# Kernel optimization log

Measured on AMD Instinct MI355X. Metric: run time of the kernel, lower is better.

The kernel has to match this reference:

```python
import jax, jax.numpy as jnp
import numpy as np

N = 32768      # total nodes = 256 graphs x 128 nodes
G = 256        # graphs in batch
NPG = 128      # nodes per graph
DEG = 8        # incoming edges per node
E = N * DEG    # 262144 edges
F_IN = 64      # node feature size
F_E = 16       # edge feature size
EMB = 64       # out_channels per head == embedding_size
H = 4          # attention heads
HC = H * EMB   # 256
DENSE = 256
K = 64         # ceil(0.5 * NPG)
EPS = 1e-5


def setup_inputs() -> dict:
    key = jax.random.key(0)
    ks = list(jax.random.split(key, 32))
    it = iter(ks)
    s = 0.05

    def rn(shape):
        return jax.random.normal(next(it), shape, jnp.float32) * s

    x = jax.random.normal(next(it), (N, F_IN), jnp.float32)
    dst = jnp.repeat(jnp.arange(N, dtype=jnp.int32), DEG)
    src = (dst // NPG) * NPG + jax.random.randint(next(it), (E,), 0, NPG, dtype=jnp.int32)
    edge_index = jnp.stack([src, dst])                      # [2, E], edges stay within graph
    edge_attr = jax.random.normal(next(it), (E, F_E), jnp.float32)
    batch_index = jnp.arange(N, dtype=jnp.int32) // NPG

    inp = dict(
        x=x, edge_index=edge_index, edge_attr=edge_attr, batch_index=batch_index,
        # TransformerConv 1 (in=F_IN)
        Wq1=rn((F_IN, HC)), bq1=jnp.zeros((HC,), jnp.float32),
        Wk1=rn((F_IN, HC)), bk1=jnp.zeros((HC,), jnp.float32),
        Wv1=rn((F_IN, HC)), bv1=jnp.zeros((HC,), jnp.float32),
        We1=rn((F_E, HC)),
        Ws1=rn((F_IN, HC)), bs1=jnp.zeros((HC,), jnp.float32),
        Wb1=rn((3 * HC, 1)),
        t1_W=rn((HC, EMB)), t1_b=jnp.zeros((EMB,), jnp.float32),
        bn1_g=jnp.ones((EMB,), jnp.float32), bn1_b=jnp.zeros((EMB,), jnp.float32),
        # TransformerConv 2 (in=EMB)
        Wq2=rn((EMB, HC)), bq2=jnp.zeros((HC,), jnp.float32),
        Wk2=rn((EMB, HC)), bk2=jnp.zeros((HC,), jnp.float32),
        Wv2=rn((EMB, HC)), bv2=jnp.zeros((HC,), jnp.float32),
        We2=rn((F_E, HC)),
        Ws2=rn((EMB, HC)), bs2=jnp.zeros((HC,), jnp.float32),
        Wb2=rn((3 * HC, 1)),
        t2_W=rn((HC, EMB)), t2_b=jnp.zeros((EMB,), jnp.float32),
        bn2_g=jnp.ones((EMB,), jnp.float32), bn2_b=jnp.zeros((EMB,), jnp.float32),
        # TopKPooling + MLP head
        pool_w=rn((EMB,)),
        l1_W=rn((2 * EMB, DENSE)), l1_b=jnp.zeros((DENSE,), jnp.float32),
        l2_W=rn((DENSE, DENSE // 2)), l2_b=jnp.zeros((DENSE // 2,), jnp.float32),
        l3_W=rn((DENSE // 2, 1)), l3_b=jnp.zeros((1,), jnp.float32),
    )
    return inp


def _tconv(x, src, dst, ea, Wq, bq, Wk, bk, Wv, bv, We, Ws, bs, Wb):
    """PyG TransformerConv with edge_dim, beta=True, concat=True."""
    n = x.shape[0]
    q = (x @ Wq + bq).reshape(n, H, EMB)                    # [N,H,C]
    eemb = (ea @ We).reshape(-1, H, EMB)                    # [E,H,C]
    k = (x @ Wk + bk)[src].reshape(-1, H, EMB) + eemb       # edge features added to key
    v = (x @ Wv + bv)[src].reshape(-1, H, EMB) + eemb       # and to value
    alpha = jnp.einsum('ehc,ehc->eh', q[dst], k) / jnp.sqrt(jnp.float32(EMB))  # [E,H]
    # stable segment softmax over incoming edges of each dst node
    amax = jax.ops.segment_max(alpha, dst, num_segments=n)
    pexp = jnp.exp(alpha - amax[dst])
    denom = jax.ops.segment_sum(pexp, dst, num_segments=n)
    attn = pexp / denom[dst]                                # [E,H]
    out = jax.ops.segment_sum(v * attn[..., None], dst, num_segments=n).reshape(n, HC)
    # beta gated skip: lin_skip(x) and lin_beta([out, xr, out-xr])
    xr = x @ Ws + bs
    beta = jax.nn.sigmoid(jnp.concatenate([out, xr, out - xr], axis=-1) @ Wb)  # [N,1]
    return beta * xr + (1.0 - beta) * out


def _bn(x, g, b):
    m = x.mean(0)
    v = x.var(0)
    return g * (x - m) * jax.lax.rsqrt(v + EPS) + b


def _forward(x, edge_attr,
             Wq1, bq1, Wk1, bk1, Wv1, bv1, We1, Ws1, bs1, Wb1, t1_W, t1_b, bn1_g, bn1_b,
             Wq2, bq2, Wk2, bk2, Wv2, bv2, We2, Ws2, bs2, Wb2, t2_W, t2_b, bn2_g, bn2_b,
             pool_w, l1_W, l1_b, l2_W, l2_b, l3_W, l3_b,
             edge_index, batch_index):
    src, dst = edge_index[0], edge_index[1]
    h = _tconv(x, src, dst, edge_attr, Wq1, bq1, Wk1, bk1, Wv1, bv1, We1, Ws1, bs1, Wb1)
    h = _bn(jax.nn.relu(h @ t1_W + t1_b), bn1_g, bn1_b)
    h = _tconv(h, src, dst, edge_attr, Wq2, bq2, Wk2, bk2, Wv2, bv2, We2, Ws2, bs2, Wb2)
    h = _bn(jax.nn.relu(h @ t2_W + t2_b), bn2_g, bn2_b)
    # TopKPooling: score = (x.w)/||w||, keep top K per graph, scale by tanh(score)
    score = (h @ pool_w) / jnp.linalg.norm(pool_w)          # [N]
    sv, si = jax.lax.top_k(score.reshape(G, NPG), K)        # [G,K]
    xs = jnp.take_along_axis(h.reshape(G, NPG, EMB), si[..., None], axis=1)  # [G,K,EMB]
    xs = xs * jnp.tanh(sv)[..., None]
    # readout: global max pool || global mean pool
    rep = jnp.concatenate([xs.max(axis=1), xs.mean(axis=1)], axis=-1)  # [G, 2*EMB]
    hd = jax.nn.relu(rep @ l1_W + l1_b)
    hd = jax.nn.relu(hd @ l2_W + l2_b)
    return hd @ l3_W + l3_b                                  # [G,1]


def reference(x, edge_index, edge_attr, batch_index,
              Wq1, bq1, Wk1, bk1, Wv1, bv1, We1, Ws1, bs1, Wb1, t1_W, t1_b, bn1_g, bn1_b,
              Wq2, bq2, Wk2, bk2, Wv2, bv2, We2, Ws2, bs2, Wb2, t2_W, t2_b, bn2_g, bn2_b,
              pool_w, l1_W, l1_b, l2_W, l2_b, l3_W, l3_b):
    return _forward(x, edge_attr,
                    Wq1, bq1, Wk1, bk1, Wv1, bv1, We1, Ws1, bs1, Wb1, t1_W, t1_b, bn1_g, bn1_b,
                    Wq2, bq2, Wk2, bk2, Wv2, bv2, We2, Ws2, bs2, Wb2, t2_W, t2_b, bn2_g, bn2_b,
                    pool_w, l1_W, l1_b, l2_W, l2_b, l3_W, l3_b,
                    edge_index, batch_index)
```

## Files before the change

### kernel.cpp

```cpp
#include <hip/hip_runtime.h>
#include <math.h>

#define NN 32768
#define NG 256
#define DEG 8
#define HC 256
#define NCAT 1088
#define HCP 320
#define KTOP 64
#define EPSBN 1e-5f

typedef __attribute__((ext_vector_type(8))) short short8v;
typedef __attribute__((ext_vector_type(4))) float f32x4;

__device__ inline float bf2f(unsigned short u) {
    union { unsigned int i; float f; } c; c.i = ((unsigned int)u) << 16; return c.f;
}
__device__ inline unsigned short f2bf(float f) {
    union { float f; unsigned int i; } c; c.f = f;
    unsigned int r = c.i + 0x7FFFu + ((c.i >> 16) & 1u);
    return (unsigned short)(r >> 16);
}
__device__ inline void split2(float v, unsigned short& hi, unsigned short& lo) {
    hi = f2bf(v);
    union { float f; unsigned int i; } c; c.f = v - bf2f(hi);
    lo = (unsigned short)(c.i >> 16);
}
__device__ inline int permcol(int n) {
    if (n < 256 || n >= 768) return n;
    if (n < 512) { int l = n - 256; return 256 + ((l >> 2) << 3) + (l & 3); }
    int l = n - 512; return 256 + ((l >> 2) << 3) + 4 + (l & 3);
}

__device__ void prep_dev(int b, int t,
    const float* __restrict__ Wq, const float* __restrict__ bq,
    const float* __restrict__ Wk, const float* __restrict__ bk,
    const float* __restrict__ Wv, const float* __restrict__ bv,
    const float* __restrict__ Ws, const float* __restrict__ bs,
    const float* __restrict__ We, const float* __restrict__ tW,
    const float* __restrict__ Wb,
    unsigned short* __restrict__ WThi, unsigned short* __restrict__ WTlo,
    float* __restrict__ bcat,
    unsigned short* __restrict__ tWThi, unsigned short* __restrict__ tWTlo,
    float* __restrict__ Wbf, float* __restrict__ stats)
{
    if (b < 16) {
        int n = b * 64 + (t >> 2);
        int cc = n & 255;
        const float* src = (n < 256) ? Wq : (n < 512) ? Wk : (n < 768) ? Wv : Ws;
        int p = permcol(n);
        int k0 = (t & 3) * 16;
        #pragma unroll
        for (int k = k0; k < k0 + 16; k++) {
            unsigned short h, l;
            split2(src[k * 256 + cc], h, l);
            WThi[p * 64 + k] = h; WTlo[p * 64 + k] = l;
        }
    } else if (b < 32) {
        int idx = (b - 16) * 256 + t;
        int k = idx >> 6, o = idx & 63;
        int h = o >> 4, f = o & 15;
        const float* wq = Wq + k * 256 + h * 64;
        const float* we = We + f * 256 + h * 64;
        float s = 0.f;
        #pragma unroll
        for (int d = 0; d < 64; d++) s += wq[d] * we[d];
        unsigned short hh, ll;
        split2(s, hh, ll);
        WThi[(1024 + o) * 64 + k] = hh; WTlo[(1024 + o) * 64 + k] = ll;
    } else if (b < 48) {
        int idx = (b - 32) * 256 + t;
        int kp = idx >> 6, n = idx & 63;
        int h = kp >> 4, f = kp & 15;
        const float* we = We + f * 256 + h * 64;
        const float* tw = tW + (h * 64) * 64 + n;
        float s = 0.f;
        #pragma unroll
        for (int d = 0; d < 64; d++) s += we[d] * tw[d * 64];
        unsigned short hh, ll;
        split2(s, hh, ll);
        tWThi[n * HCP + 256 + kp] = hh; tWTlo[n * HCP + 256 + kp] = ll;
    } else if (b < 64) {
        int base = (b - 48) * 1024 + t * 4;
        #pragma unroll
        for (int i = 0; i < 4; i++) {
            int idx = base + i;
            int n = idx >> 8, k = idx & 255;
            unsigned short h, l;
            split2(tW[k * 64 + n], h, l);
            tWThi[n * HCP + k] = h; tWTlo[n * HCP + k] = l;
        }
    } else {
        if (t < 128) stats[t] = 0.f;
        Wbf[t]       = Wb[t]       + Wb[512 + t];
        Wbf[256 + t] = Wb[256 + t] - Wb[512 + t];
        for (int c = t; c < 1024; c += 256) {
            int cc = c & 255;
            float v = (c < 256) ? bq[cc] : (c < 512) ? bk[cc] : (c < 768) ? bv[cc] : bs[cc];
            bcat[permcol(c)] = v;
        }
        if (t < 64) {
            int h = t >> 4, f = t & 15;
            const float* we = We + f * 256 + h * 64;
            float s = 0.f, sb = 0.f;
            #pragma unroll
            for (int d = 0; d < 64; d++) {
                s  += we[d] * (Wb[h * 64 + d] + Wb[512 + h * 64 + d]);
                sb += we[d] * bq[h * 64 + d];
            }
            Wbf[512 + t] = s;
            bcat[1024 + t] = sb;
        }
    }
}

__global__ __launch_bounds__(256) void prep_all(
    const float* Wq1, const float* bq1, const float* Wk1, const float* bk1,
    const float* Wv1, const float* bv1, const float* Ws1, const float* bs1,
    const float* We1, const float* t1W, const float* Wb1,
    unsigned short* WThi1, unsigned short* WTlo1, float* bcat1,
    unsigned short* tWThi1, unsigned short* tWTlo1, float* Wbf1, float* stats1,
    const float* Wq2, const float* bq2, const float* Wk2, const float* bk2,
    const float* Wv2, const float* bv2, const float* Ws2, const float* bs2,
    const float* We2, const float* t2W, const float* Wb2,
    unsigned short* WThi2, unsigned short* WTlo2, float* bcat2,
    unsigned short* tWThi2, unsigned short* tWTlo2, float* Wbf2, float* stats2)
{
    const int b = blockIdx.x, t = threadIdx.x;
    if (b < 65)
        prep_dev(b, t, Wq1, bq1, Wk1, bk1, Wv1, bv1, Ws1, bs1, We1, t1W, Wb1,
                 WThi1, WTlo1, bcat1, tWThi1, tWTlo1, Wbf1, stats1);
    else
        prep_dev(b - 65, t, Wq2, bq2, Wk2, bk2, Wv2, bv2, Ws2, bs2, We2, t2W, Wb2,
                 WThi2, WTlo2, bcat2, tWThi2, tWTlo2, Wbf2, stats2);
}

__global__ __launch_bounds__(256) void proj_mfma(
    const float* __restrict__ A, const float* __restrict__ stats,
    const float* __restrict__ gbn, const float* __restrict__ bbn,
    const unsigned short* __restrict__ WThi, const unsigned short* __restrict__ WTlo,
    const float* __restrict__ bcat, unsigned short* __restrict__ C)
{
    __shared__ unsigned short AhiL[4096], AloL[4096];
    __shared__ unsigned short WhiL[4096], WloL[4096];
    __shared__ float CL[64 * 68];
    __shared__ float scl[64], sft[64];
    const int t = threadIdx.x;
    const int row0 = blockIdx.x * 64;
    const int w = t >> 6, l = t & 63;
    const int lr = l & 15, lg = l >> 4, ls = l & 7;

    if (t < 64) {
        if (stats) {
            float mean = stats[t] * (1.f / NN);
            float var  = stats[64 + t] * (1.f / NN) - mean * mean;
            float s = gbn[t] * rsqrtf(var + EPSBN);
            scl[t] = s; sft[t] = bbn[t] - mean * s;
        } else { scl[t] = 1.f; sft[t] = 0.f; }
    }
    __syncthreads();

    #pragma unroll
    for (int g = 0; g < 2; g++) {
        int idx = t * 8 + g * 2048;
        int r = idx >> 6, c = idx & 63;
        int ch = (c >> 3) ^ (r & 7);
        float4 a0 = *(const float4*)(A + (size_t)(row0 + r) * 64 + c);
        float4 a1 = *(const float4*)(A + (size_t)(row0 + r) * 64 + c + 4);
        float av[8] = {a0.x, a0.y, a0.z, a0.w, a1.x, a1.y, a1.z, a1.w};
        short8v vh, vl;
        #pragma unroll
        for (int j = 0; j < 8; j++) {
            float v = av[j] * scl[c + j] + sft[c + j];
            unsigned short h2, l2;
            split2(v, h2, l2);
            vh[j] = (short)h2; vl[j] = (short)l2;
        }
        *(short8v*)(AhiL + r * 64 + ch * 8) = vh;
        *(short8v*)(AloL + r * 64 + ch * 8) = vl;
    }

    for (int n0 = 0; n0 < NCAT; n0 += 64) {
        #pragma unroll
        for (int g = 0; g < 2; g++) {
            int idx = t * 8 + g * 2048;
            int r = idx >> 6, c = idx & 63;
            int ch = (c >> 3) ^ (r & 7);
            *(short8v*)(WhiL + r * 64 + ch * 8) =
                *(const short8v*)(WThi + (size_t)(n0 + r) * 64 + c);
            *(short8v*)(WloL + r * 64 + ch * 8) =
                *(const short8v*)(WTlo + (size_t)(n0 + r) * 64 + c);
        }
        __syncthreads();
        f32x4 acc[4] = {};
        #pragma unroll
        for (int kk = 0; kk < 2; kk++) {
            int ch = (kk * 4 + lg) ^ ls;
            short8v ah = *(short8v*)(AhiL + (w * 16 + lr) * 64 + ch * 8);
            short8v al = *(short8v*)(AloL + (w * 16 + lr) * 64 + ch * 8);
            #pragma unroll
            for (int nt = 0; nt < 4; nt++) {
                short8v bh = *(short8v*)(WhiL + (nt * 16 + lr) * 64 + ch * 8);
                short8v bl = *(short8v*)(WloL + (nt * 16 + lr) * 64 + ch * 8);
                acc[nt] = __builtin_amdgcn_mfma_f32_16x16x32_bf16(ah, bh, acc[nt], 0, 0, 0);
                acc[nt] = __builtin_amdgcn_mfma_f32_16x16x32_bf16(al, bh, acc[nt], 0, 0, 0);
                acc[nt] = __builtin_amdgcn_mfma_f32_16x16x32_bf16(ah, bl, acc[nt], 0, 0, 0);
            }
        }
        #pragma unroll
        for (int nt = 0; nt < 4; nt++)
            #pragma unroll
            for (int r = 0; r < 4; r++)
                CL[(w * 16 + lg * 4 + r) * 68 + nt * 16 + lr] = acc[nt][r];
        __syncthreads();
        {
            int r = t >> 2, cb = (t & 3) * 16;
            #pragma unroll
            for (int jj = 0; jj < 2; jj++) {
                f32x4 p0 = *(f32x4*)(CL + r * 68 + cb + jj * 8);
                f32x4 p1 = *(f32x4*)(CL + r * 68 + cb + jj * 8 + 4);
                float4 b0 = *(const float4*)(bcat + n0 + cb + jj * 8);
                float4 b1 = *(const float4*)(bcat + n0 + cb + jj * 8 + 4);
                short8v o;
                o[0] = (short)f2bf(p0[0] + b0.x); o[1] = (short)f2bf(p0[1] + b0.y);
                o[2] = (short)f2bf(p0[2] + b0.z); o[3] = (short)f2bf(p0[3] + b0.w);
                o[4] = (short)f2bf(p1[0] + b1.x); o[5] = (short)f2bf(p1[1] + b1.y);
                o[6] = (short)f2bf(p1[2] + b1.z); o[7] = (short)f2bf(p1[3] + b1.w);
                *(short8v*)(C + (size_t)(row0 + r) * NCAT + n0 + cb + jj * 8) = o;
            }
        }
        __syncthreads();
    }
}

__global__ __launch_bounds__(256) void gemm_t(
    const unsigned short* __restrict__ Ahi, const unsigned short* __restrict__ Alo,
    const unsigned short* __restrict__ WThi, const unsigned short* __restrict__ WTlo,
    const float* __restrict__ bias, float* __restrict__ Tout,
    float* __restrict__ stats)
{
    __shared__ char smem[32768];
    unsigned short* AhiL = (unsigned short*)smem;
    unsigned short* AloL = AhiL + 4096;
    unsigned short* WhiL = AloL + 4096;
    unsigned short* WloL = WhiL + 4096;
    float* CL = (float*)smem;
    const int t = threadIdx.x;
    const int row0 = blockIdx.x * 64;
    const int w = t >> 6, l = t & 63;
    const int lr = l & 15, lg = l >> 4, ls = l & 7;
    f32x4 acc[4] = {};
    for (int kt = 0; kt < 5; kt++) {
        if (kt) __syncthreads();
        #pragma unroll
        for (int g = 0; g < 2; g++) {
            int idx = t * 8 + g * 2048;
            int r = idx >> 6, c = idx & 63;
            int ch = (c >> 3) ^ (r & 7);
            *(short8v*)(AhiL + r * 64 + ch * 8) =
                *(const short8v*)(Ahi + (size_t)(row0 + r) * HCP + kt * 64 + c);
            *(short8v*)(AloL + r * 64 + ch * 8) =
                *(const short8v*)(Alo + (size_t)(row0 + r) * HCP + kt * 64 + c);
            *(short8v*)(WhiL + r * 64 + ch * 8) =
                *(const short8v*)(WThi + r * HCP + kt * 64 + c);
            *(short8v*)(WloL + r * 64 + ch * 8) =
                *(const short8v*)(WTlo + r * HCP + kt * 64 + c);
        }
        __syncthreads();
        #pragma unroll
        for (int kk = 0; kk < 2; kk++) {
            int ch = (kk * 4 + lg) ^ ls;
            short8v ah = *(short8v*)(AhiL + (w * 16 + lr) * 64 + ch * 8);
            short8v al = *(short8v*)(AloL + (w * 16 + lr) * 64 + ch * 8);
            #pragma unroll
            for (int nt = 0; nt < 4; nt++) {
                short8v bh = *(short8v*)(WhiL + (nt * 16 + lr) * 64 + ch * 8);
                short8v bl = *(short8v*)(WloL + (nt * 16 + lr) * 64 + ch * 8);
                acc[nt] = __builtin_amdgcn_mfma_f32_16x16x32_bf16(ah, bh, acc[nt], 0, 0, 0);
                acc[nt] = __builtin_amdgcn_mfma_f32_16x16x32_bf16(al, bh, acc[nt], 0, 0, 0);
                acc[nt] = __builtin_amdgcn_mfma_f32_16x16x32_bf16(ah, bl, acc[nt], 0, 0, 0);
            }
        }
    }
    __syncthreads();
    #pragma unroll
    for (int nt = 0; nt < 4; nt++)
        #pragma unroll
        for (int r = 0; r < 4; r++)
            CL[(w * 16 + lg * 4 + r) * 68 + nt * 16 + lr] = acc[nt][r];
    __syncthreads();
    {
        int r = t >> 2, cb = (t & 3) * 16;
        #pragma unroll
        for (int jj = 0; jj < 4; jj++) {
            f32x4 p = *(f32x4*)(CL + r * 68 + cb + jj * 4);
            float4 bb = *(const float4*)(bias + cb + jj * 4);
            float4 o;
            o.x = fmaxf(p[0] + bb.x, 0.f); o.y = fmaxf(p[1] + bb.y, 0.f);
            o.z = fmaxf(p[2] + bb.z, 0.f); o.w = fmaxf(p[3] + bb.w, 0.f);
            *(float4*)(Tout + (size_t)(row0 + r) * 64 + cb + jj * 4) = o;
        }
    }
    if (t < 64) {
        float bb = bias[t];
        float s = 0.f, s2 = 0.f;
        #pragma unroll 8
        for (int r = 0; r < 64; r++) {
            float v = fmaxf(CL[r * 68 + t] + bb, 0.f);
            s += v; s2 += v * v;
        }
        atomicAdd(&stats[t], s);
        atomicAdd(&stats[64 + t], s2);
    }
}

__global__ __launch_bounds__(256, 6) void attn_fused(
    const unsigned short* __restrict__ C,
    const float* __restrict__ Wbf,
    const int* __restrict__ srcIdx, const float* __restrict__ EA,
    unsigned short* __restrict__ Hhi, unsigned short* __restrict__ Hlo)
{
    const int t = threadIdx.x;
    const int lane = t & 63;
    const int wave = t >> 6;
    const int bid = blockIdx.x;
    const int swz = (bid & 7) * 1024 + (bid >> 3);
    const int n = swz * 4 + wave;
    const int c0 = lane * 4;
    const int h = lane >> 4;
    const int fi = lane & 15;

    const unsigned short* rowN = C + (size_t)n * NCAT;
    ushort4 qv = *(const ushort4*)(rowN + c0);
    float q0 = bf2f(qv.x), q1 = bf2f(qv.y), q2 = bf2f(qv.z), q3 = bf2f(qv.w);
    float qe_l = bf2f(rowN[1024 + h * 16 + fi]);

    const int ebase = n * DEG;
    int sj = srcIdx[ebase + (lane & 7)];
    int ss[DEG];
    #pragma unroll
    for (int j = 0; j < DEG; j++) ss[j] = __shfl(sj, j);

    short8v kv[DEG];
    float eav[DEG];
    #pragma unroll
    for (int j = 0; j < DEG; j++) {
        kv[j] = *(const short8v*)(C + (size_t)ss[j] * NCAT + 256 + lane * 8);
        eav[j] = EA[(size_t)(ebase + j) * 16 + fi];
    }
    float alpha[DEG];
    #pragma unroll
    for (int j = 0; j < DEG; j++) {
        float d = eav[j] * qe_l
                + q0 * bf2f((unsigned short)kv[j][0]) + q1 * bf2f((unsigned short)kv[j][1])
                + q2 * bf2f((unsigned short)kv[j][2]) + q3 * bf2f((unsigned short)kv[j][3]);
        d += __shfl_xor(d, 1); d += __shfl_xor(d, 2);
        d += __shfl_xor(d, 4); d += __shfl_xor(d, 8);
        alpha[j] = d * 0.125f;
    }
    float mx = alpha[0];
    #pragma unroll
    for (int j = 1; j < DEG; j++) mx = fmaxf(mx, alpha[j]);
    float wsum = 0.f;
    #pragma unroll
    for (int j = 0; j < DEG; j++) { alpha[j] = expf(alpha[j] - mx); wsum += alpha[j]; }
    float inv = 1.f / wsum;

    float o0 = 0.f, o1 = 0.f, o2 = 0.f, o3 = 0.f, eg = 0.f;
    #pragma unroll
    for (int j = 0; j < DEG; j++) {
        float wj = alpha[j] * inv;
        eg += wj * eav[j];
        o0 += wj * bf2f((unsigned short)kv[j][4]);
        o1 += wj * bf2f((unsigned short)kv[j][5]);
        o2 += wj * bf2f((unsigned short)kv[j][6]);
        o3 += wj * bf2f((unsigned short)kv[j][7]);
    }

    ushort4 sv = *(const ushort4*)(rowN + 768 + c0);
    float xr0 = bf2f(sv.x), xr1 = bf2f(sv.y), xr2 = bf2f(sv.z), xr3 = bf2f(sv.w);

    float part = eg * Wbf[512 + lane];
    {
        f32x4 w13 = *(const f32x4*)(Wbf + c0);
        f32x4 w23 = *(const f32x4*)(Wbf + 256 + c0);
        part += o0 * w13[0] + o1 * w13[1] + o2 * w13[2] + o3 * w13[3];
        part += xr0 * w23[0] + xr1 * w23[1] + xr2 * w23[2] + xr3 * w23[3];
    }
    part += __shfl_xor(part, 1);  part += __shfl_xor(part, 2);
    part += __shfl_xor(part, 4);  part += __shfl_xor(part, 8);
    part += __shfl_xor(part, 16); part += __shfl_xor(part, 32);
    float beta = 1.f / (1.f + expf(-part));
    float omb = 1.f - beta;

    ushort4 hh, hl;
    split2(beta * xr0 + omb * o0, hh.x, hl.x);
    split2(beta * xr1 + omb * o1, hh.y, hl.y);
    split2(beta * xr2 + omb * o2, hh.z, hl.z);
    split2(beta * xr3 + omb * o3, hh.w, hl.w);
    *(ushort4*)(Hhi + (size_t)n * HCP + c0) = hh;
    *(ushort4*)(Hlo + (size_t)n * HCP + c0) = hl;

    unsigned short zh, zl;
    split2(omb * eg, zh, zl);
    Hhi[(size_t)n * HCP + 256 + lane] = zh;
    Hlo[(size_t)n * HCP + 256 + lane] = zl;
}

__global__ __launch_bounds__(128) void pool_mlp(
    const float* __restrict__ Hn, const float* __restrict__ stats,
    const float* __restrict__ gbn, const float* __restrict__ bbn,
    const float* __restrict__ pw,
    const float* __restrict__ W1, const float* __restrict__ b1,
    const float* __restrict__ W2, const float* __restrict__ b2,
    const float* __restrict__ W3, const float* __restrict__ b3,
    float* __restrict__ out)
{
    __shared__ float sh[128][65];
    __shared__ float spw[64];
    __shared__ float sc[128];
    __shared__ float sscale[128];
    __shared__ int   skeep[128];
    __shared__ float rmax[2][64], rsum[2][64];
    __shared__ float srep[128];
    __shared__ float sh1[256];
    __shared__ float sh2[128];
    __shared__ float wred[2];
    __shared__ float scl[64], sft[64];
    const int g = blockIdx.x, t = threadIdx.x;

    if (t < 64) {
        float mean = stats[t] * (1.f / NN);
        float var  = stats[64 + t] * (1.f / NN) - mean * mean;
        float s = gbn[t] * rsqrtf(var + EPSBN);
        scl[t] = s; sft[t] = bbn[t] - mean * s;
        spw[t] = pw[t];
    }
    __syncthreads();
    for (int i = t; i < 128 * 64; i += 128) {
        int c = i & 63;
        sh[i >> 6][c] = Hn[(size_t)g * 128 * 64 + i] * scl[c] + sft[c];
    }
    __syncthreads();

    float nw = 0.f;
    #pragma unroll
    for (int i = 0; i < 64; i++) { float w = spw[i]; nw += w * w; }
    float invn = rsqrtf(nw);

    float s = 0.f;
    #pragma unroll
    for (int i = 0; i < 64; i++) s += sh[t][i] * spw[i];
    s *= invn;
    sc[t] = s;
    __syncthreads();

    int rank = 0;
    for (int m = 0; m < 128; m++) {
        float sm = sc[m];
        rank += (sm > s) || (sm == s && m < t);
    }
    skeep[t] = (rank < KTOP);
    sscale[t] = tanhf(s);
    __syncthreads();

    {
        int c = t & 63, half = t >> 6;
        float mxv = -1e30f, sm = 0.f;
        for (int r = half * 64; r < half * 64 + 64; r++) {
            if (skeep[r]) {
                float v = sh[r][c] * sscale[r];
                mxv = fmaxf(mxv, v); sm += v;
            }
        }
        rmax[half][c] = mxv; rsum[half][c] = sm;
    }
    __syncthreads();
    if (t < 64) {
        srep[t] = fmaxf(rmax[0][t], rmax[1][t]);
        srep[64 + t] = (rsum[0][t] + rsum[1][t]) * (1.f / KTOP);
    }
    __syncthreads();

    #pragma unroll
    for (int jj = 0; jj < 2; jj++) {
        int j = t + jj * 128;
        float a = b1[j];
        for (int c2 = 0; c2 < 128; c2++) a += srep[c2] * W1[c2 * 256 + j];
        sh1[j] = fmaxf(a, 0.f);
    }
    __syncthreads();
    {
        float a = b2[t];
        for (int c2 = 0; c2 < 256; c2++) a += sh1[c2] * W2[c2 * 128 + t];
        sh2[t] = fmaxf(a, 0.f);
    }
    __syncthreads();
    float p = sh2[t] * W3[t];
    p += __shfl_xor(p, 1);  p += __shfl_xor(p, 2);  p += __shfl_xor(p, 4);
    p += __shfl_xor(p, 8);  p += __shfl_xor(p, 16); p += __shfl_xor(p, 32);
    if ((t & 63) == 0) wred[t >> 6] = p;
    __syncthreads();
    if (t == 0) out[g] = wred[0] + wred[1] + b3[0];
}

extern "C" void kernel_launch(void* const* d_in, const int* in_sizes, int n_in,
                              void* d_out, int out_size, void* d_ws, size_t ws_size,
                              hipStream_t stream)
{
    const float* x    = (const float*)d_in[0];
    const int*   ei   = (const int*)  d_in[1];
    const float* ea   = (const float*)d_in[2];
    const int*   srcI = ei;
    const float* Wq1 = (const float*)d_in[4];  const float* bq1 = (const float*)d_in[5];
    const float* Wk1 = (const float*)d_in[6];  const float* bk1 = (const float*)d_in[7];
    const float* Wv1 = (const float*)d_in[8];  const float* bv1 = (const float*)d_in[9];
    const float* We1 = (const float*)d_in[10];
    const float* Ws1 = (const float*)d_in[11]; const float* bs1 = (const float*)d_in[12];
    const float* Wb1 = (const float*)d_in[13];
    const float* t1W = (const float*)d_in[14]; const float* t1b = (const float*)d_in[15];
    const float* g1  = (const float*)d_in[16]; const float* be1 = (const float*)d_in[17];
    const float* Wq2 = (const float*)d_in[18]; const float* bq2 = (const float*)d_in[19];
    const float* Wk2 = (const float*)d_in[20]; const float* bk2 = (const float*)d_in[21];
    const float* Wv2 = (const float*)d_in[22]; const float* bv2 = (const float*)d_in[23];
    const float* We2 = (const float*)d_in[24];
    const float* Ws2 = (const float*)d_in[25]; const float* bs2 = (const float*)d_in[26];
    const float* Wb2 = (const float*)d_in[27];
    const float* t2W = (const float*)d_in[28]; const float* t2b = (const float*)d_in[29];
    const float* g2  = (const float*)d_in[30]; const float* be2 = (const float*)d_in[31];
    const float* pw  = (const float*)d_in[32];
    const float* l1W = (const float*)d_in[33]; const float* l1b = (const float*)d_in[34];
    const float* l2W = (const float*)d_in[35]; const float* l2b = (const float*)d_in[36];
    const float* l3W = (const float*)d_in[37]; const float* l3b = (const float*)d_in[38];

    char* ws = (char*)d_ws;
    unsigned short* C   = (unsigned short*)ws;
    unsigned short* Hhi = (unsigned short*)(ws + (size_t)NN * NCAT * 2);
    unsigned short* Hlo = Hhi + (size_t)NN * HCP;
    float* bT   = (float*)(Hlo + (size_t)NN * HCP);
    float* bT2  = bT + (size_t)NN * 64;
    float* bcat1  = bT2 + (size_t)NN * 64;
    float* bcat2  = bcat1 + NCAT;
    float* stats1 = bcat2 + NCAT;
    float* stats2 = stats1 + 128;
    float* Wbf1   = stats2 + 128;
    float* Wbf2   = Wbf1 + 576;
    unsigned short* WThi1  = (unsigned short*)(Wbf2 + 576);
    unsigned short* WTlo1  = WThi1 + (size_t)NCAT * 64;
    unsigned short* WThi2  = WTlo1 + (size_t)NCAT * 64;
    unsigned short* WTlo2  = WThi2 + (size_t)NCAT * 64;
    unsigned short* tWThi1 = WTlo2 + (size_t)NCAT * 64;
    unsigned short* tWTlo1 = tWThi1 + 64 * HCP;
    unsigned short* tWThi2 = tWTlo1 + 64 * HCP;
    unsigned short* tWTlo2 = tWThi2 + 64 * HCP;

    const dim3 blk(256);

    prep_all<<<130, blk, 0, stream>>>(
        Wq1, bq1, Wk1, bk1, Wv1, bv1, Ws1, bs1, We1, t1W, Wb1,
        WThi1, WTlo1, bcat1, tWThi1, tWTlo1, Wbf1, stats1,
        Wq2, bq2, Wk2, bk2, Wv2, bv2, Ws2, bs2, We2, t2W, Wb2,
        WThi2, WTlo2, bcat2, tWThi2, tWTlo2, Wbf2, stats2);

    proj_mfma<<<512, blk, 0, stream>>>(x, nullptr, nullptr, nullptr,
                                       WThi1, WTlo1, bcat1, C);
    attn_fused<<<NN / 4, blk, 0, stream>>>(C, Wbf1, srcI, ea, Hhi, Hlo);
    gemm_t<<<512, blk, 0, stream>>>(Hhi, Hlo, tWThi1, tWTlo1, t1b, bT, stats1);

    proj_mfma<<<512, blk, 0, stream>>>(bT, stats1, g1, be1,
                                       WThi2, WTlo2, bcat2, C);
    attn_fused<<<NN / 4, blk, 0, stream>>>(C, Wbf2, srcI, ea, Hhi, Hlo);
    gemm_t<<<512, blk, 0, stream>>>(Hhi, Hlo, tWThi2, tWTlo2, t2b, bT2, stats2);

    pool_mlp<<<NG, 128, 0, stream>>>(bT2, stats2, g2, be2, pw,
                                     l1W, l1b, l2W, l2b, l3W, l3b,
                                     (float*)d_out);
}
```

Measured before the change: 201.9 us.

## Split projection GEMM over a 2D grid of column tiles and use fast exp/rcp

```diff
diff --git a/kernel.cpp b/kernel.cpp
--- a/kernel.cpp
+++ b/kernel.cpp
@@ -141,12 +141,16 @@
     const unsigned short* __restrict__ WThi, const unsigned short* __restrict__ WTlo,
     const float* __restrict__ bcat, unsigned short* __restrict__ C)
 {
-    __shared__ unsigned short AhiL[4096], AloL[4096];
-    __shared__ unsigned short WhiL[4096], WloL[4096];
-    __shared__ float CL[64 * 68];
+    __shared__ char smem[32768];
+    unsigned short* AhiL = (unsigned short*)smem;
+    unsigned short* AloL = AhiL + 4096;
+    unsigned short* WhiL = AloL + 4096;
+    unsigned short* WloL = WhiL + 4096;
+    float* CL = (float*)smem;
     __shared__ float scl[64], sft[64];
     const int t = threadIdx.x;
-    const int row0 = blockIdx.x * 64;
+    const int n0 = blockIdx.x * 64;
+    const int row0 = blockIdx.y * 64;
     const int w = t >> 6, l = t & 63;
     const int lr = l & 15, lg = l >> 4, ls = l & 7;
 
@@ -178,58 +182,50 @@
         }
         *(short8v*)(AhiL + r * 64 + ch * 8) = vh;
         *(short8v*)(AloL + r * 64 + ch * 8) = vl;
-    }
-
-    for (int n0 = 0; n0 < NCAT; n0 += 64) {
-        #pragma unroll
-        for (int g = 0; g < 2; g++) {
-            int idx = t * 8 + g * 2048;
-            int r = idx >> 6, c = idx & 63;
-            int ch = (c >> 3) ^ (r & 7);
-            *(short8v*)(WhiL + r * 64 + ch * 8) =
-                *(const short8v*)(WThi + (size_t)(n0 + r) * 64 + c);
-            *(short8v*)(WloL + r * 64 + ch * 8) =
-                *(const short8v*)(WTlo + (size_t)(n0 + r) * 64 + c);
-        }
-        __syncthreads();
-        f32x4 acc[4] = {};
-        #pragma unroll
-        for (int kk = 0; kk < 2; kk++) {
-            int ch = (kk * 4 + lg) ^ ls;
-            short8v ah = *(short8v*)(AhiL + (w * 16 + lr) * 64 + ch * 8);
-            short8v al = *(short8v*)(AloL + (w * 16 + lr) * 64 + ch * 8);
-            #pragma unroll
-            for (int nt = 0; nt < 4; nt++) {
-                short8v bh = *(short8v*)(WhiL + (nt * 16 + lr) * 64 + ch * 8);
-                short8v bl = *(short8v*)(WloL + (nt * 16 + lr) * 64 + ch * 8);
-                acc[nt] = __builtin_amdgcn_mfma_f32_16x16x32_bf16(ah, bh, acc[nt], 0, 0, 0);
-                acc[nt] = __builtin_amdgcn_mfma_f32_16x16x32_bf16(al, bh, acc[nt], 0, 0, 0);
-                acc[nt] = __builtin_amdgcn_mfma_f32_16x16x32_bf16(ah, bl, acc[nt], 0, 0, 0);
-            }
-        }
-        #pragma unroll
-        for (int nt = 0; nt < 4; nt++)
-            #pragma unroll
-            for (int r = 0; r < 4; r++)
-                CL[(w * 16 + lg * 4 + r) * 68 + nt * 16 + lr] = acc[nt][r];
-        __syncthreads();
-        {
-            int r = t >> 2, cb = (t & 3) * 16;
-            #pragma unroll
-            for (int jj = 0; jj < 2; jj++) {
-                f32x4 p0 = *(f32x4*)(CL + r * 68 + cb + jj * 8);
-                f32x4 p1 = *(f32x4*)(CL + r * 68 + cb + jj * 8 + 4);
-                float4 b0 = *(const float4*)(bcat + n0 + cb + jj * 8);
-                float4 b1 = *(const float4*)(bcat + n0 + cb + jj * 8 + 4);
-                short8v o;
-                o[0] = (short)f2bf(p0[0] + b0.x); o[1] = (short)f2bf(p0[1] + b0.y);
-                o[2] = (short)f2bf(p0[2] + b0.z); o[3] = (short)f2bf(p0[3] + b0.w);
-                o[4] = (short)f2bf(p1[0] + b1.x); o[5] = (short)f2bf(p1[1] + b1.y);
-                o[6] = (short)f2bf(p1[2] + b1.z); o[7] = (short)f2bf(p1[3] + b1.w);
-                *(short8v*)(C + (size_t)(row0 + r) * NCAT + n0 + cb + jj * 8) = o;
-            }
-        }
-        __syncthreads();
+        *(short8v*)(WhiL + r * 64 + ch * 8) =
+            *(const short8v*)(WThi + (size_t)(n0 + r) * 64 + c);
+        *(short8v*)(WloL + r * 64 + ch * 8) =
+            *(const short8v*)(WTlo + (size_t)(n0 + r) * 64 + c);
+    }
+    __syncthreads();
+
+    f32x4 acc[4] = {};
+    #pragma unroll
+    for (int kk = 0; kk < 2; kk++) {
+        int ch = (kk * 4 + lg) ^ ls;
+        short8v ah = *(short8v*)(AhiL + (w * 16 + lr) * 64 + ch * 8);
+        short8v al = *(short8v*)(AloL + (w * 16 + lr) * 64 + ch * 8);
+        #pragma unroll
+        for (int nt = 0; nt < 4; nt++) {
+            short8v bh = *(short8v*)(WhiL + (nt * 16 + lr) * 64 + ch * 8);
+            short8v bl = *(short8v*)(WloL + (nt * 16 + lr) * 64 + ch * 8);
+            acc[nt] = __builtin_amdgcn_mfma_f32_16x16x32_bf16(ah, bh, acc[nt], 0, 0, 0);
+            acc[nt] = __builtin_amdgcn_mfma_f32_16x16x32_bf16(al, bh, acc[nt], 0, 0, 0);
+            acc[nt] = __builtin_amdgcn_mfma_f32_16x16x32_bf16(ah, bl, acc[nt], 0, 0, 0);
+        }
+    }
+    __syncthreads();
+    #pragma unroll
+    for (int nt = 0; nt < 4; nt++)
+        #pragma unroll
+        for (int r = 0; r < 4; r++)
+            CL[(w * 16 + lg * 4 + r) * 68 + nt * 16 + lr] = acc[nt][r];
+    __syncthreads();
+    {
+        int r = t >> 2, cb = (t & 3) * 16;
+        #pragma unroll
+        for (int jj = 0; jj < 2; jj++) {
+            f32x4 p0 = *(f32x4*)(CL + r * 68 + cb + jj * 8);
+            f32x4 p1 = *(f32x4*)(CL + r * 68 + cb + jj * 8 + 4);
+            float4 b0 = *(const float4*)(bcat + n0 + cb + jj * 8);
+            float4 b1 = *(const float4*)(bcat + n0 + cb + jj * 8 + 4);
+            short8v o;
+            o[0] = (short)f2bf(p0[0] + b0.x); o[1] = (short)f2bf(p0[1] + b0.y);
+            o[2] = (short)f2bf(p0[2] + b0.z); o[3] = (short)f2bf(p0[3] + b0.w);
+            o[4] = (short)f2bf(p1[0] + b1.x); o[5] = (short)f2bf(p1[1] + b1.y);
+            o[6] = (short)f2bf(p1[2] + b1.z); o[7] = (short)f2bf(p1[3] + b1.w);
+            *(short8v*)(C + (size_t)(row0 + r) * NCAT + n0 + cb + jj * 8) = o;
+        }
     }
 }
 
@@ -363,8 +359,8 @@
     for (int j = 1; j < DEG; j++) mx = fmaxf(mx, alpha[j]);
     float wsum = 0.f;
     #pragma unroll
-    for (int j = 0; j < DEG; j++) { alpha[j] = expf(alpha[j] - mx); wsum += alpha[j]; }
-    float inv = 1.f / wsum;
+    for (int j = 0; j < DEG; j++) { alpha[j] = __expf(alpha[j] - mx); wsum += alpha[j]; }
+    float inv = __builtin_amdgcn_rcpf(wsum);
 
     float o0 = 0.f, o1 = 0.f, o2 = 0.f, o3 = 0.f, eg = 0.f;
     #pragma unroll
@@ -390,7 +386,7 @@
     part += __shfl_xor(part, 1);  part += __shfl_xor(part, 2);
     part += __shfl_xor(part, 4);  part += __shfl_xor(part, 8);
     part += __shfl_xor(part, 16); part += __shfl_xor(part, 32);
-    float beta = 1.f / (1.f + expf(-part));
+    float beta = __builtin_amdgcn_rcpf(1.f + __expf(-part));
     float omb = 1.f - beta;
 
     ushort4 hh, hl;
@@ -555,6 +551,7 @@
     unsigned short* tWTlo2 = tWThi2 + 64 * HCP;
 
     const dim3 blk(256);
+    const dim3 gProj(17, 512);
 
     prep_all<<<130, blk, 0, stream>>>(
         Wq1, bq1, Wk1, bk1, Wv1, bv1, Ws1, bs1, We1, t1W, Wb1,
@@ -562,13 +559,13 @@
         Wq2, bq2, Wk2, bk2, Wv2, bv2, Ws2, bs2, We2, t2W, Wb2,
         WThi2, WTlo2, bcat2, tWThi2, tWTlo2, Wbf2, stats2);
 
-    proj_mfma<<<512, blk, 0, stream>>>(x, nullptr, nullptr, nullptr,
-                                       WThi1, WTlo1, bcat1, C);
+    proj_mfma<<<gProj, blk, 0, stream>>>(x, nullptr, nullptr, nullptr,
+                                         WThi1, WTlo1, bcat1, C);
     attn_fused<<<NN / 4, blk, 0, stream>>>(C, Wbf1, srcI, ea, Hhi, Hlo);
     gemm_t<<<512, blk, 0, stream>>>(Hhi, Hlo, tWThi1, tWTlo1, t1b, bT, stats1);
 
-    proj_mfma<<<512, blk, 0, stream>>>(bT, stats1, g1, be1,
-                                       WThi2, WTlo2, bcat2, C);
+    proj_mfma<<<gProj, blk, 0, stream>>>(bT, stats1, g1, be1,
+                                         WThi2, WTlo2, bcat2, C);
     attn_fused<<<NN / 4, blk, 0, stream>>>(C, Wbf2, srcI, ea, Hhi, Hlo);
     gemm_t<<<512, blk, 0, stream>>>(Hhi, Hlo, tWThi2, tWTlo2, t2b, bT2, stats2);
 
```

Result: faster. 193.7 us, median of 2 (-4.1%).
